# Optimization experiments

Hardware: AMD Instinct MI355X
Metric: run time of the kernel (lower is better)

Reference implementation:

```python
import jax, jax.numpy as jnp
import numpy as np

B, N, C, H, W = 32, 32, 3, 32, 32
HID, OUT = 256, 128


def _conv(x, w, b):
    y = jax.lax.conv_general_dilated(
        x, w, window_strides=(1, 1), padding="SAME",
        dimension_numbers=("NCHW", "OIHW", "NCHW"))
    return y + b[None, :, None, None]


def _sage(h, lw, lb, rw):
    # PyG SAGEConv with mean aggregation on a fully-connected graph (no self-loops):
    # agg_i = (sum_j h_j - h_i) / (N-1); out = agg @ lw.T + lb + h @ rw.T
    n = h.shape[1]
    agg = (jnp.sum(h, axis=1, keepdims=True) - h) / (n - 1)
    return jnp.einsum('bnd,od->bno', agg, lw) + lb + jnp.einsum('bnd,od->bno', h, rw)


def setup_inputs() -> dict:
    key = jax.random.key(0)
    ks = jax.random.split(key, 16)
    def g(k, shape, scale):
        return jax.random.normal(k, shape, dtype=jnp.float32) * scale
    return {
        "x": jax.random.normal(ks[0], (B, N, C, H, W), dtype=jnp.float32),
        "mask": jnp.ones((B, N), dtype=jnp.float32),
        "conv1_w": g(ks[1], (64, C, 3, 3), 0.1),
        "conv1_b": jnp.zeros((64,), jnp.float32),
        "conv2_w": g(ks[2], (128, 64, 3, 3), 0.05),
        "conv2_b": jnp.zeros((128,), jnp.float32),
        "fc_w": g(ks[3], (HID, 128), 0.08),
        "fc_b": jnp.zeros((HID,), jnp.float32),
        "s1_lw": g(ks[4], (HID, HID), 0.06),
        "s1_lb": jnp.zeros((HID,), jnp.float32),
        "s1_rw": g(ks[5], (HID, HID), 0.06),
        "s2_lw": g(ks[6], (OUT, HID), 0.06),
        "s2_lb": jnp.zeros((OUT,), jnp.float32),
        "s2_rw": g(ks[7], (OUT, HID), 0.06),
    }


def reference(x, mask, conv1_w, conv1_b, conv2_w, conv2_b, fc_w, fc_b,
              s1_lw, s1_lb, s1_rw, s2_lw, s2_lb, s2_rw):
    b, n, c, h, w = x.shape
    z = x.reshape(b * n, c, h, w)
    z = jax.nn.relu(_conv(z, conv1_w, conv1_b))
    z = jax.nn.relu(_conv(z, conv2_w, conv2_b))
    z = jnp.mean(z, axis=(2, 3))                      # AdaptiveAvgPool2d((1,1)) + flatten
    z = z @ fc_w.T + fc_b                             # [B*N, HID]
    z = z.reshape(b, n, -1) * mask[:, :, None]
    z = jax.nn.relu(_sage(z, s1_lw, s1_lb, s1_rw))
    z = _sage(z, s2_lw, s2_lb, s2_rw)                 # [B, N, OUT]
    return z
```

## Files before the change

kernel.cpp:

```cpp
#include <hip/hip_runtime.h>
#include <hip/hip_bf16.h>


typedef __attribute__((ext_vector_type(8))) short bfrag;
typedef __attribute__((ext_vector_type(4))) float f32x4;

static __device__ __forceinline__ unsigned short f2bf(float f) {
    union { float f; unsigned u; } v; v.f = f;
    unsigned r = v.u + 0x7fff + ((v.u >> 16) & 1);
    return (unsigned short)(r >> 16);
}

__global__ __launch_bounds__(256) void prep_kernel(
    const float* __restrict__ s1lw, const float* __restrict__ s1rw,
    const float* __restrict__ s2lw, const float* __restrict__ s2rw,
    const float* __restrict__ c2w, const float* __restrict__ c1w,
    const float* __restrict__ c1b, const float* __restrict__ fcw,
    float* __restrict__ l1T, float* __restrict__ w1pT,
    float* __restrict__ l2T, float* __restrict__ w2pT,
    float* __restrict__ fwT,
    short* __restrict__ w2b, short* __restrict__ w1b) {
    int i = blockIdx.x * 256 + threadIdx.x;
    const float inv31 = 1.f / 31.f;
    if (i < 65536) {
        int d = i >> 8, o = i & 255;
        float lw = s1lw[o * 256 + d];
        l1T[i]  = lw;
        w1pT[i] = s1rw[o * 256 + d] - lw * inv31;
    }
    if (i < 32768) {
        int d = i >> 7, o = i & 127;
        float lw = s2lw[o * 256 + d];
        l2T[i]  = lw;
        w2pT[i] = s2rw[o * 256 + d] - lw * inv31;
        int c = i >> 8, o2 = i & 255;
        fwT[i] = fcw[o2 * 128 + c];
    }
    if (i < 73728) {
        int k = i >> 13, rem = i & 8191, oc = rem >> 6, ic = rem & 63;
        w2b[i] = (short)f2bf(c2w[(oc * 64 + ic) * 9 + k]);
    }
    if (i < 2048) {
        int oc = i >> 5, k = i & 31;
        float v = (k < 27) ? c1w[oc * 27 + k] : (k == 27 ? c1b[oc] : 0.f);
        w1b[i] = (short)f2bf(v);
    }
}

__global__ __launch_bounds__(256, 2) void fused_conv_kernel(
    const float* __restrict__ x, const short* __restrict__ w1b,
    const short* __restrict__ w2b, const float* __restrict__ b2,
    float* __restrict__ pooled4) {
    const int band = blockIdx.x, img = blockIdx.y;
    __shared__ short xt[3 * 12 * 34];
    __shared__ short c1t[10 * 34 * 72];
    __shared__ float wsum[4][64];
    const int t = threadIdx.x;
    const int w = t >> 6, lane = t & 63;
    const int ln15 = lane & 15, q8 = (lane >> 4) * 8;
    const int rg2 = w & 1, og = w >> 1;

    const float* xi = x + img * 3072;
    for (int idx = t; idx < 1224; idx += 256) {
        int c = idx / 408, rem = idx % 408, r = rem / 34, col = rem % 34;
        int y = band * 8 - 2 + r, xx = col - 1;
        float v = 0.f;
        if ((unsigned)y < 32u && (unsigned)xx < 32u) v = xi[c * 1024 + y * 32 + xx];
        xt[idx] = (short)f2bf(v);
    }
    {
        f32x4 z = {0.f, 0.f, 0.f, 0.f};
        for (int i = t; i < 180; i += 256) {
            int r = i / 18, rem = i % 18, side = rem / 9, q = rem % 9;
            *(f32x4*)(c1t + (r * 34 + side * 33) * 72 + q * 8) = z;
        }
    }
    bfrag b1f[4];
#pragma unroll
    for (int ot = 0; ot < 4; ++ot)
        b1f[ot] = *(const bfrag*)(w1b + (ot * 16 + ln15) * 32 + q8);
    __syncthreads();

#pragma unroll 1
    for (int pt = 0; pt < 5; ++pt) {
        const int tile = w * 5 + pt;
        const int posA = tile * 16 + ln15;
        const int baseA = (posA >> 5) * 34 + (posA & 31);
        bfrag a1f;
#pragma unroll
        for (int j = 0; j < 8; ++j) {
            int k = q8 + j;
            int c = (k * 57) >> 9;
            int rem = k - 9 * c;
            int dy = (rem * 11) >> 5;
            int dx = rem - 3 * dy;
            int cc = c < 3 ? c : 2;
            short v = xt[cc * 408 + baseA + dy * 34 + dx];
            if (c >= 3) v = (k == 27) ? (short)0x3F80 : (short)0;
            a1f[j] = v;
        }
        f32x4 acc1[4];
#pragma unroll
        for (int ot = 0; ot < 4; ++ot) {
#pragma unroll
            for (int rg = 0; rg < 4; ++rg) acc1[ot][rg] = 0.f;
            acc1[ot] = __builtin_amdgcn_mfma_f32_16x16x32_bf16(
                a1f, b1f[ot], acc1[ot], 0, 0, 0);
        }
#pragma unroll
        for (int rg = 0; rg < 4; ++rg) {
            int pos = tile * 16 + (lane >> 4) * 4 + rg;
            int r = pos >> 5, xc = pos & 31;
            int y = band * 8 - 1 + r;
            bool valid = (unsigned)y < 32u;
#pragma unroll
            for (int ot = 0; ot < 4; ++ot) {
                float v = fmaxf(acc1[ot][rg], 0.f);
                c1t[(r * 34 + xc + 1) * 72 + ot * 16 + ln15] =
                    valid ? (short)f2bf(v) : (short)0;
            }
        }
    }
    __syncthreads();

    float b2v[4];
#pragma unroll
    for (int ot = 0; ot < 4; ++ot) b2v[ot] = b2[og * 64 + ot * 16 + ln15];

    f32x4 acc[8][4];
#pragma unroll
    for (int pt = 0; pt < 8; ++pt)
#pragma unroll
        for (int ot = 0; ot < 4; ++ot)
#pragma unroll
            for (int rg = 0; rg < 4; ++rg) acc[pt][ot][rg] = 0.f;

    int aBase[8];
#pragma unroll
    for (int pt = 0; pt < 8; ++pt) {
        int r = rg2 * 4 + (pt >> 1);
        int xc = ((pt & 1) << 4) + ln15;
        aBase[pt] = (r * 34 + xc) * 72 + q8;
    }

    const short* wb0 = w2b + (og * 64 + ln15) * 64 + q8;
    auto loadB = [&](bfrag* dst, int tap) {
        const short* p = wb0 + tap * 8192;
#pragma unroll
        for (int kc = 0; kc < 2; ++kc)
#pragma unroll
            for (int ot = 0; ot < 4; ++ot)
                dst[kc * 4 + ot] = *(const bfrag*)(p + ot * 1024 + kc * 32);
    };
    auto compute = [&](const bfrag* bf, int tap) {
        const int dy = tap / 3, dx = tap - dy * 3;
        const int dOff = (dy * 34 + dx) * 72;
#pragma unroll
        for (int pt = 0; pt < 8; ++pt) {
            const int a0 = aBase[pt] + dOff;
#pragma unroll
            for (int kc = 0; kc < 2; ++kc) {
                bfrag a2f = *(const bfrag*)(&c1t[a0 + kc * 32]);
#pragma unroll
                for (int ot = 0; ot < 4; ++ot)
                    acc[pt][ot] = __builtin_amdgcn_mfma_f32_16x16x32_bf16(
                        a2f, bf[kc * 4 + ot], acc[pt][ot], 0, 0, 0);
            }
        }
    };

    bfrag bA[8], bB[8];
    loadB(bA, 0);
#pragma unroll 1
    for (int tap = 0; tap < 9; tap += 2) {
        if (tap + 1 < 9) loadB(bB, tap + 1);
        compute(bA, tap);
        if (tap + 2 < 9) loadB(bA, tap + 2);
        if (tap + 1 < 9) compute(bB, tap + 1);
    }

#pragma unroll
    for (int ot = 0; ot < 4; ++ot) {
        float s = 0.f;
#pragma unroll
        for (int pt = 0; pt < 8; ++pt)
#pragma unroll
            for (int rg = 0; rg < 4; ++rg)
                s += fmaxf(acc[pt][ot][rg] + b2v[ot], 0.f);
        s += __shfl_xor(s, 16, 64);
        s += __shfl_xor(s, 32, 64);
        if (lane < 16) wsum[w][ot * 16 + ln15] = s;
    }
    __syncthreads();
    if (t < 128) {
        int og2 = t >> 6, oo = t & 63;
        pooled4[((size_t)img * 4 + band) * 128 + t] =
            wsum[og2 * 2][oo] + wsum[og2 * 2 + 1][oo];
    }
}

__global__ __launch_bounds__(256) void fc_kernel(
    const float* __restrict__ pooled4, const float* __restrict__ fwT,
    const float* __restrict__ fb, const float* __restrict__ mask,
    float* __restrict__ z1) {
    const int img = blockIdx.x;
    __shared__ float m[128];
    const int t = threadIdx.x;
    if (t < 128) {
        const float* p = pooled4 + (size_t)img * 4 * 128 + t;
        m[t] = (p[0] + p[128] + p[256] + p[384]) * (1.f / 1024.f);
    }
    __syncthreads();
    float acc = fb[t];
#pragma unroll 4
    for (int c = 0; c < 128; ++c) acc = fmaf(m[c], fwT[c * 256 + t], acc);
    z1[img * 256 + t] = acc * mask[img];
}

__global__ __launch_bounds__(256) void sage1_kernel(
    const float* __restrict__ z1, const float* __restrict__ l1T,
    const float* __restrict__ lb, const float* __restrict__ w1pT,
    float* __restrict__ z2) {
    const int bb = blockIdx.x >> 3, chunk = blockIdx.x & 7;
    __shared__ float h[32 * 256];
    __shared__ float sl[256];
    const int t = threadIdx.x;
    const float* zb = z1 + bb * 8192;
    for (int idx = t; idx < 8192; idx += 256) h[idx] = zb[idx];
    __syncthreads();
    float s = 0.f;
#pragma unroll
    for (int n = 0; n < 32; ++n) s += h[n * 256 + t];
    sl[t] = s * (1.f / 31.f);
    __syncthreads();
    float c = lb[t];
#pragma unroll 4
    for (int d = 0; d < 256; ++d) c = fmaf(sl[d], l1T[d * 256 + t], c);
    float acc[4];
#pragma unroll
    for (int i = 0; i < 4; ++i) acc[i] = c;
    for (int d0 = 0; d0 < 256; d0 += 4) {
        float wv0 = w1pT[(d0 + 0) * 256 + t];
        float wv1 = w1pT[(d0 + 1) * 256 + t];
        float wv2 = w1pT[(d0 + 2) * 256 + t];
        float wv3 = w1pT[(d0 + 3) * 256 + t];
#pragma unroll
        for (int i = 0; i < 4; ++i) {
            f32x4 hv = *(const f32x4*)&h[(chunk * 4 + i) * 256 + d0];
            acc[i] = fmaf(hv[0], wv0, acc[i]);
            acc[i] = fmaf(hv[1], wv1, acc[i]);
            acc[i] = fmaf(hv[2], wv2, acc[i]);
            acc[i] = fmaf(hv[3], wv3, acc[i]);
        }
    }
    for (int i = 0; i < 4; ++i)
        z2[(bb * 32 + chunk * 4 + i) * 256 + t] = fmaxf(acc[i], 0.f);
}

__global__ __launch_bounds__(256) void sage2_kernel(
    const float* __restrict__ z2, const float* __restrict__ l2T,
    const float* __restrict__ lb, const float* __restrict__ w2pT,
    float* __restrict__ out) {
    const int bb = blockIdx.x >> 3, chunk = blockIdx.x & 7;
    __shared__ float h[32 * 256];
    __shared__ float sl[256];
    const int t = threadIdx.x;
    const float* zb = z2 + bb * 8192;
    for (int idx = t; idx < 8192; idx += 256) h[idx] = zb[idx];
    __syncthreads();
    float s = 0.f;
#pragma unroll
    for (int n = 0; n < 32; ++n) s += h[n * 256 + t];
    sl[t] = s * (1.f / 31.f);
    __syncthreads();
    const int o = t & 127, half = t >> 7;
    float c = lb[o];
#pragma unroll 4
    for (int d = 0; d < 256; ++d) c = fmaf(sl[d], l2T[d * 128 + o], c);
    float acc[2];
    acc[0] = c; acc[1] = c;
    const int n0 = chunk * 4 + half * 2;
    for (int d0 = 0; d0 < 256; d0 += 4) {
        float wv0 = w2pT[(d0 + 0) * 128 + o];
        float wv1 = w2pT[(d0 + 1) * 128 + o];
        float wv2 = w2pT[(d0 + 2) * 128 + o];
        float wv3 = w2pT[(d0 + 3) * 128 + o];
#pragma unroll
        for (int ii = 0; ii < 2; ++ii) {
            f32x4 hv = *(const f32x4*)&h[(n0 + ii) * 256 + d0];
            acc[ii] = fmaf(hv[0], wv0, acc[ii]);
            acc[ii] = fmaf(hv[1], wv1, acc[ii]);
            acc[ii] = fmaf(hv[2], wv2, acc[ii]);
            acc[ii] = fmaf(hv[3], wv3, acc[ii]);
        }
    }
    for (int ii = 0; ii < 2; ++ii)
        out[(size_t)(bb * 32 + n0 + ii) * 128 + o] = acc[ii];
}

extern "C" void kernel_launch(void* const* d_in, const int* in_sizes, int n_in,
                              void* d_out, int out_size, void* d_ws, size_t ws_size,
                              hipStream_t stream) {
    const float* x    = (const float*)d_in[0];
    const float* mask = (const float*)d_in[1];
    const float* c1w  = (const float*)d_in[2];
    const float* c1b  = (const float*)d_in[3];
    const float* c2w  = (const float*)d_in[4];
    const float* c2b  = (const float*)d_in[5];
    const float* fcw  = (const float*)d_in[6];
    const float* fcb  = (const float*)d_in[7];
    const float* s1lw = (const float*)d_in[8];
    const float* s1lb = (const float*)d_in[9];
    const float* s1rw = (const float*)d_in[10];
    const float* s2lw = (const float*)d_in[11];
    const float* s2lb = (const float*)d_in[12];
    const float* s2rw = (const float*)d_in[13];
    float* out = (float*)d_out;

    char* ws = (char*)d_ws;
    float* pooled4 = (float*)(ws);
    float* z1      = (float*)(ws + 2048u * 1024);
    float* z2      = (float*)(ws + 3072u * 1024);
    float* l1T     = (float*)(ws + 4096u * 1024);
    float* w1pT    = (float*)(ws + 4352u * 1024);
    float* l2T     = (float*)(ws + 4608u * 1024);
    float* w2pT    = (float*)(ws + 4736u * 1024);
    float* fwT     = (float*)(ws + 4864u * 1024);
    short* w2b     = (short*)(ws + 4992u * 1024);
    short* w1b     = (short*)(ws + 5136u * 1024);

    prep_kernel<<<dim3(288), 256, 0, stream>>>(s1lw, s1rw, s2lw, s2rw, c2w, c1w, c1b,
                                               fcw, l1T, w1pT, l2T, w2pT, fwT, w2b, w1b);
    fused_conv_kernel<<<dim3(4, 1024), 256, 0, stream>>>(x, w1b, w2b, c2b, pooled4);
    fc_kernel<<<dim3(1024), 256, 0, stream>>>(pooled4, fwT, fcb, mask, z1);
    sage1_kernel<<<dim3(256), 256, 0, stream>>>(z1, l1T, s1lb, w1pT, z2);
    sage2_kernel<<<dim3(256), 256, 0, stream>>>(z2, l2T, s2lb, w2pT, out);
}
```

Before: 309.8 us.

## Fuse fc, sage1 and sage2 into one tail kernel per graph

Replaces the three tail kernels (fc, sage1, sage2) with one kernel launched once per graph chunk. Each block recomputes the fc output and the first SAGE layer for all 32 nodes of its graph in shared memory, then does its slice of the second SAGE layer. This removes two launches and the z1/z2 global round trips. In exchange each of the 8 blocks per graph repeats the fc and sage1 work (8x redundant compute), uses about 70KB of shared memory, and holds 32 accumulators per thread.

```diff
diff --git a/kernel.cpp b/kernel.cpp
--- a/kernel.cpp
+++ b/kernel.cpp
@@ -199,103 +199,111 @@
     }
 }
 
-__global__ __launch_bounds__(256) void fc_kernel(
+__global__ __launch_bounds__(256) void tail_kernel(
     const float* __restrict__ pooled4, const float* __restrict__ fwT,
     const float* __restrict__ fb, const float* __restrict__ mask,
-    float* __restrict__ z1) {
-    const int img = blockIdx.x;
-    __shared__ float m[128];
-    const int t = threadIdx.x;
-    if (t < 128) {
-        const float* p = pooled4 + (size_t)img * 4 * 128 + t;
-        m[t] = (p[0] + p[128] + p[256] + p[384]) * (1.f / 1024.f);
-    }
-    __syncthreads();
-    float acc = fb[t];
-#pragma unroll 4
-    for (int c = 0; c < 128; ++c) acc = fmaf(m[c], fwT[c * 256 + t], acc);
-    z1[img * 256 + t] = acc * mask[img];
-}
-
-__global__ __launch_bounds__(256) void sage1_kernel(
-    const float* __restrict__ z1, const float* __restrict__ l1T,
-    const float* __restrict__ lb, const float* __restrict__ w1pT,
-    float* __restrict__ z2) {
-    const int bb = blockIdx.x >> 3, chunk = blockIdx.x & 7;
-    __shared__ float h[32 * 256];
-    __shared__ float sl[256];
-    const int t = threadIdx.x;
-    const float* zb = z1 + bb * 8192;
-    for (int idx = t; idx < 8192; idx += 256) h[idx] = zb[idx];
-    __syncthreads();
-    float s = 0.f;
-#pragma unroll
-    for (int n = 0; n < 32; ++n) s += h[n * 256 + t];
-    sl[t] = s * (1.f / 31.f);
-    __syncthreads();
-    float c = lb[t];
-#pragma unroll 4
-    for (int d = 0; d < 256; ++d) c = fmaf(sl[d], l1T[d * 256 + t], c);
-    float acc[4];
-#pragma unroll
-    for (int i = 0; i < 4; ++i) acc[i] = c;
-    for (int d0 = 0; d0 < 256; d0 += 4) {
-        float wv0 = w1pT[(d0 + 0) * 256 + t];
-        float wv1 = w1pT[(d0 + 1) * 256 + t];
-        float wv2 = w1pT[(d0 + 2) * 256 + t];
-        float wv3 = w1pT[(d0 + 3) * 256 + t];
-#pragma unroll
-        for (int i = 0; i < 4; ++i) {
-            f32x4 hv = *(const f32x4*)&h[(chunk * 4 + i) * 256 + d0];
-            acc[i] = fmaf(hv[0], wv0, acc[i]);
-            acc[i] = fmaf(hv[1], wv1, acc[i]);
-            acc[i] = fmaf(hv[2], wv2, acc[i]);
-            acc[i] = fmaf(hv[3], wv3, acc[i]);
-        }
-    }
-    for (int i = 0; i < 4; ++i)
-        z2[(bb * 32 + chunk * 4 + i) * 256 + t] = fmaxf(acc[i], 0.f);
-}
-
-__global__ __launch_bounds__(256) void sage2_kernel(
-    const float* __restrict__ z2, const float* __restrict__ l2T,
-    const float* __restrict__ lb, const float* __restrict__ w2pT,
+    const float* __restrict__ l1T, const float* __restrict__ lb1,
+    const float* __restrict__ w1pT, const float* __restrict__ l2T,
+    const float* __restrict__ lb2, const float* __restrict__ w2pT,
     float* __restrict__ out) {
     const int bb = blockIdx.x >> 3, chunk = blockIdx.x & 7;
-    __shared__ float h[32 * 256];
+    __shared__ float m[32 * 128];
+    __shared__ float hA[32 * 256];
+    __shared__ float hB[32 * 256];
     __shared__ float sl[256];
+    __shared__ float mk[32];
     const int t = threadIdx.x;
-    const float* zb = z2 + bb * 8192;
-    for (int idx = t; idx < 8192; idx += 256) h[idx] = zb[idx];
-    __syncthreads();
-    float s = 0.f;
-#pragma unroll
-    for (int n = 0; n < 32; ++n) s += h[n * 256 + t];
-    sl[t] = s * (1.f / 31.f);
-    __syncthreads();
-    const int o = t & 127, half = t >> 7;
-    float c = lb[o];
+    if (t < 32) mk[t] = mask[bb * 32 + t];
+    for (int idx = t; idx < 4096; idx += 256) {
+        int n = idx >> 7, c = idx & 127;
+        const float* p = pooled4 + ((size_t)(bb * 32 + n) * 4) * 128 + c;
+        m[idx] = (p[0] + p[128] + p[256] + p[384]) * (1.f / 1024.f);
+    }
+    __syncthreads();
+    float acc[32];
+#pragma unroll
+    for (int n = 0; n < 32; ++n) acc[n] = 0.f;
+    for (int c0 = 0; c0 < 128; c0 += 4) {
+        float wv0 = fwT[(c0 + 0) * 256 + t];
+        float wv1 = fwT[(c0 + 1) * 256 + t];
+        float wv2 = fwT[(c0 + 2) * 256 + t];
+        float wv3 = fwT[(c0 + 3) * 256 + t];
+#pragma unroll
+        for (int n = 0; n < 32; ++n) {
+            f32x4 hv = *(const f32x4*)&m[n * 128 + c0];
+            acc[n] = fmaf(hv[0], wv0, acc[n]);
+            acc[n] = fmaf(hv[1], wv1, acc[n]);
+            acc[n] = fmaf(hv[2], wv2, acc[n]);
+            acc[n] = fmaf(hv[3], wv3, acc[n]);
+        }
+    }
+    {
+        float fbv = fb[t];
+        for (int n = 0; n < 32; ++n) hA[n * 256 + t] = (acc[n] + fbv) * mk[n];
+    }
+    __syncthreads();
+    {
+        float s = 0.f;
+#pragma unroll
+        for (int n = 0; n < 32; ++n) s += hA[n * 256 + t];
+        sl[t] = s * (1.f / 31.f);
+    }
+    __syncthreads();
+    {
+        float c1v = lb1[t];
 #pragma unroll 4
-    for (int d = 0; d < 256; ++d) c = fmaf(sl[d], l2T[d * 128 + o], c);
-    float acc[2];
-    acc[0] = c; acc[1] = c;
-    const int n0 = chunk * 4 + half * 2;
-    for (int d0 = 0; d0 < 256; d0 += 4) {
-        float wv0 = w2pT[(d0 + 0) * 128 + o];
-        float wv1 = w2pT[(d0 + 1) * 128 + o];
-        float wv2 = w2pT[(d0 + 2) * 128 + o];
-        float wv3 = w2pT[(d0 + 3) * 128 + o];
-#pragma unroll
-        for (int ii = 0; ii < 2; ++ii) {
-            f32x4 hv = *(const f32x4*)&h[(n0 + ii) * 256 + d0];
-            acc[ii] = fmaf(hv[0], wv0, acc[ii]);
-            acc[ii] = fmaf(hv[1], wv1, acc[ii]);
-            acc[ii] = fmaf(hv[2], wv2, acc[ii]);
-            acc[ii] = fmaf(hv[3], wv3, acc[ii]);
-        }
-    }
-    for (int ii = 0; ii < 2; ++ii)
-        out[(size_t)(bb * 32 + n0 + ii) * 128 + o] = acc[ii];
+        for (int d = 0; d < 256; ++d) c1v = fmaf(sl[d], l1T[d * 256 + t], c1v);
+#pragma unroll
+        for (int n = 0; n < 32; ++n) acc[n] = c1v;
+        for (int d0 = 0; d0 < 256; d0 += 4) {
+            float wv0 = w1pT[(d0 + 0) * 256 + t];
+            float wv1 = w1pT[(d0 + 1) * 256 + t];
+            float wv2 = w1pT[(d0 + 2) * 256 + t];
+            float wv3 = w1pT[(d0 + 3) * 256 + t];
+#pragma unroll
+            for (int n = 0; n < 32; ++n) {
+                f32x4 hv = *(const f32x4*)&hA[n * 256 + d0];
+                acc[n] = fmaf(hv[0], wv0, acc[n]);
+                acc[n] = fmaf(hv[1], wv1, acc[n]);
+                acc[n] = fmaf(hv[2], wv2, acc[n]);
+                acc[n] = fmaf(hv[3], wv3, acc[n]);
+            }
+        }
+        for (int n = 0; n < 32; ++n) hB[n * 256 + t] = fmaxf(acc[n], 0.f);
+    }
+    __syncthreads();
+    {
+        float s = 0.f;
+#pragma unroll
+        for (int n = 0; n < 32; ++n) s += hB[n * 256 + t];
+        sl[t] = s * (1.f / 31.f);
+    }
+    __syncthreads();
+    {
+        const int o = t & 127, half = t >> 7;
+        float c2v = lb2[o];
+#pragma unroll 4
+        for (int d = 0; d < 256; ++d) c2v = fmaf(sl[d], l2T[d * 128 + o], c2v);
+        float a2[2];
+        a2[0] = c2v; a2[1] = c2v;
+        const int n0 = chunk * 4 + half * 2;
+        for (int d0 = 0; d0 < 256; d0 += 4) {
+            float wv0 = w2pT[(d0 + 0) * 128 + o];
+            float wv1 = w2pT[(d0 + 1) * 128 + o];
+            float wv2 = w2pT[(d0 + 2) * 128 + o];
+            float wv3 = w2pT[(d0 + 3) * 128 + o];
+#pragma unroll
+            for (int ii = 0; ii < 2; ++ii) {
+                f32x4 hv = *(const f32x4*)&hB[(n0 + ii) * 256 + d0];
+                a2[ii] = fmaf(hv[0], wv0, a2[ii]);
+                a2[ii] = fmaf(hv[1], wv1, a2[ii]);
+                a2[ii] = fmaf(hv[2], wv2, a2[ii]);
+                a2[ii] = fmaf(hv[3], wv3, a2[ii]);
+            }
+        }
+        for (int ii = 0; ii < 2; ++ii)
+            out[(size_t)(bb * 32 + n0 + ii) * 128 + o] = a2[ii];
+    }
 }
 
 extern "C" void kernel_launch(void* const* d_in, const int* in_sizes, int n_in,
@@ -319,8 +327,6 @@
 
     char* ws = (char*)d_ws;
     float* pooled4 = (float*)(ws);
-    float* z1      = (float*)(ws + 2048u * 1024);
-    float* z2      = (float*)(ws + 3072u * 1024);
     float* l1T     = (float*)(ws + 4096u * 1024);
     float* w1pT    = (float*)(ws + 4352u * 1024);
     float* l2T     = (float*)(ws + 4608u * 1024);
@@ -332,7 +338,6 @@
     prep_kernel<<<dim3(288), 256, 0, stream>>>(s1lw, s1rw, s2lw, s2rw, c2w, c1w, c1b,
                                                fcw, l1T, w1pT, l2T, w2pT, fwT, w2b, w1b);
     fused_conv_kernel<<<dim3(4, 1024), 256, 0, stream>>>(x, w1b, w2b, c2b, pooled4);
-    fc_kernel<<<dim3(1024), 256, 0, stream>>>(pooled4, fwT, fcb, mask, z1);
-    sage1_kernel<<<dim3(256), 256, 0, stream>>>(z1, l1T, s1lb, w1pT, z2);
-    sage2_kernel<<<dim3(256), 256, 0, stream>>>(z2, l2T, s2lb, w2pT, out);
-}
+    tail_kernel<<<dim3(256), 256, 0, stream>>>(pooled4, fwT, fcb, mask,
+                                               l1T, s1lb, w1pT, l2T, s2lb, w2pT, out);
+}
```

Measured after the change: 336.5 us. 8.6% more time.
